# Kernel tuning notes

Measured on AMD Instinct MI355X. Metric: run time of the kernel, lower is better.

## Reference

```python
import jax, jax.numpy as jnp
import numpy as np
import math

B, T, C = 2, 2048, 768
NH, HD = 12, 64  # n_head, head_dim

def setup_inputs() -> dict:
    key = jax.random.key(0)
    k1, k2, k3 = jax.random.split(key, 3)
    x = jax.random.normal(k1, (B, T, C), dtype=jnp.float32)
    mask = jnp.tril(jnp.ones((T, T), dtype=bool))[None, None]  # [1,1,T,T] causal
    Wqkv = jax.random.normal(k2, (C, 3 * C), dtype=jnp.float32) * (1.0 / math.sqrt(C))
    Wproj = jax.random.normal(k3, (C, C), dtype=jnp.float32) * (1.0 / math.sqrt(C))
    return {"x": x, "mask": mask, "Wqkv": Wqkv, "Wproj": Wproj}

def reference(x, mask, Wqkv, Wproj):
    b, t, c = x.shape
    qkv = x @ Wqkv  # [b,t,3c]
    q, k, v = jnp.split(qkv, 3, axis=-1)
    q = q.reshape(b, t, NH, HD).transpose(0, 2, 1, 3)  # [b,h,t,d]
    k = k.reshape(b, t, NH, HD).transpose(0, 2, 1, 3)
    v = v.reshape(b, t, NH, HD).transpose(0, 2, 1, 3)
    att = jnp.einsum('bhqd,bhkd->bhqk', q, k) / math.sqrt(HD)
    att = jnp.where(mask, att, -jnp.inf)
    att = jax.nn.softmax(att, axis=-1)
    out = jnp.einsum('bhqk,bhkd->bhqd', att, v)
    out = out.transpose(0, 2, 1, 3).reshape(b, t, c)
    return out @ Wproj
```

## Files before the change

### kernel.cpp

```cpp
#include <hip/hip_runtime.h>
#include <hip/hip_bf16.h>

#define T_   2048
#define C_   768
#define NH_  12
#define HD_  64
#define M_   (2*T_)
#define N1_  (3*C_)
#define PB_  ((size_t)NH_*T_*HD_)
#define KS_  0.180336880f
#define MK_  8.65617024f

typedef __attribute__((ext_vector_type(8))) short  short8;
typedef __attribute__((ext_vector_type(4))) short  shortx4;
typedef __attribute__((ext_vector_type(4))) float  floatx4;

__device__ __forceinline__ floatx4 mfma_bf16(short8 a, short8 b, floatx4 c) {
    return __builtin_amdgcn_mfma_f32_16x16x32_bf16(a, b, c, 0, 0, 0);
}
__device__ __forceinline__ float fast_exp2(float x) {
    return __builtin_amdgcn_exp2f(x);
}
__device__ __forceinline__ void wave_fence() {
    __builtin_amdgcn_fence(__ATOMIC_SEQ_CST, "wavefront");
}
__device__ __forceinline__ void async_load16(const __hip_bfloat16* g, __hip_bfloat16* l) {
    __builtin_amdgcn_global_load_lds(
        (const __attribute__((address_space(1))) void*)g,
        (__attribute__((address_space(3))) void*)l, 16, 0, 0);
}

__global__ __launch_bounds__(256) void prep_all(const float* __restrict__ x,
                                                const float* __restrict__ wqkv,
                                                const float* __restrict__ wproj,
                                                __hip_bfloat16* __restrict__ xb,
                                                __hip_bfloat16* __restrict__ wqkvT,
                                                __hip_bfloat16* __restrict__ wprojT) {
    if (blockIdx.x < 3072) {
        const int idx = blockIdx.x * 256 + threadIdx.x;
        const floatx4 v = ((const floatx4*)x)[idx];
        union { __hip_bfloat16 h[4]; shortx4 s; } u;
#pragma unroll
        for (int j = 0; j < 4; j++) u.h[j] = __float2bfloat16(v[j]);
        ((shortx4*)xb)[idx] = u.s;
    } else if (blockIdx.x < 3936) {
        const int j  = (blockIdx.x - 3072) * 256 + threadIdx.x;
        const int k8 = j / N1_;
        const int n  = j - k8 * N1_;
        union { __hip_bfloat16 h[8]; short8 s; } u;
#pragma unroll
        for (int jj = 0; jj < 8; jj++)
            u.h[jj] = __float2bfloat16(wqkv[(size_t)(k8 * 8 + jj) * N1_ + n]);
        *(short8*)(wqkvT + (size_t)n * C_ + k8 * 8) = u.s;
    } else {
        const int j  = (blockIdx.x - 3936) * 256 + threadIdx.x;
        const int k8 = j / C_;
        const int n  = j - k8 * C_;
        union { __hip_bfloat16 h[8]; short8 s; } u;
#pragma unroll
        for (int jj = 0; jj < 8; jj++)
            u.h[jj] = __float2bfloat16(wproj[(size_t)(k8 * 8 + jj) * C_ + n]);
        *(short8*)(wprojT + (size_t)n * C_ + k8 * 8) = u.s;
    }
}

__global__ __launch_bounds__(256) void prep1(const float* __restrict__ x,
                                             const float* __restrict__ wqkv,
                                             __hip_bfloat16* __restrict__ xb,
                                             __hip_bfloat16* __restrict__ wqkvT) {
    if (blockIdx.x < 3072) {
        const int idx = blockIdx.x * 256 + threadIdx.x;
        const floatx4 v = ((const floatx4*)x)[idx];
        union { __hip_bfloat16 h[4]; shortx4 s; } u;
#pragma unroll
        for (int j = 0; j < 4; j++) u.h[j] = __float2bfloat16(v[j]);
        ((shortx4*)xb)[idx] = u.s;
    } else {
        const int j  = (blockIdx.x - 3072) * 256 + threadIdx.x;
        const int k8 = j / N1_;
        const int n  = j - k8 * N1_;
        union { __hip_bfloat16 h[8]; short8 s; } u;
#pragma unroll
        for (int jj = 0; jj < 8; jj++)
            u.h[jj] = __float2bfloat16(wqkv[(size_t)(k8 * 8 + jj) * N1_ + n]);
        *(short8*)(wqkvT + (size_t)n * C_ + k8 * 8) = u.s;
    }
}
__global__ __launch_bounds__(256) void prep2(const float* __restrict__ wproj,
                                             __hip_bfloat16* __restrict__ wprojT) {
    const int j  = blockIdx.x * 256 + threadIdx.x;
    const int k8 = j / C_;
    const int n  = j - k8 * C_;
    union { __hip_bfloat16 h[8]; short8 s; } u;
#pragma unroll
    for (int jj = 0; jj < 8; jj++)
        u.h[jj] = __float2bfloat16(wproj[(size_t)(k8 * 8 + jj) * C_ + n]);
    *(short8*)(wprojT + (size_t)n * C_ + k8 * 8) = u.s;
}

__global__ __launch_bounds__(256) void gemm_bt64x128(const __hip_bfloat16* __restrict__ A,
                                                     const __hip_bfloat16* __restrict__ Bt,
                                                     int N, int K,
                                                     __hip_bfloat16* __restrict__ O0,
                                                     __hip_bfloat16* __restrict__ O1,
                                                     __hip_bfloat16* __restrict__ O2) {
    __shared__ __align__(16) __hip_bfloat16 As[64 * 32];
    __shared__ __align__(16) __hip_bfloat16 Bs[128 * 32];

    const int tid  = threadIdx.x;
    const int n0   = blockIdx.x * 128;
    const int m0   = blockIdx.y * 64;
    const int wave = tid >> 6;
    const int ln   = tid & 63;
    const int l16  = ln & 15;
    const int q4   = ln >> 4;
    const int wm   = (wave >> 1) * 32;
    const int wn   = (wave & 1) * 64;

    const int lrow = ln >> 2;
    const int loct = (ln & 3) * 8;
    const __hip_bfloat16* ApD  = A  + (size_t)(m0 + wave * 16 + lrow) * K + loct;
    const __hip_bfloat16* BpD0 = Bt + (size_t)(n0 + (2 * wave)     * 16 + lrow) * K + loct;
    const __hip_bfloat16* BpD1 = Bt + (size_t)(n0 + (2 * wave + 1) * 16 + lrow) * K + loct;
    __hip_bfloat16* AsD  = As + wave * 512;
    __hip_bfloat16* BsD0 = Bs + (2 * wave) * 512;
    __hip_bfloat16* BsD1 = Bs + (2 * wave + 1) * 512;

    floatx4 acc[2][4];
#pragma unroll
    for (int i = 0; i < 2; i++)
#pragma unroll
        for (int j = 0; j < 4; j++) acc[i][j] = (floatx4){0.f, 0.f, 0.f, 0.f};

    for (int k0 = 0; k0 < K; k0 += 32) {
        __syncthreads();
        async_load16(ApD  + k0, AsD);
        async_load16(BpD0 + k0, BsD0);
        async_load16(BpD1 + k0, BsD1);
        __syncthreads();
        short8 af[2], bfr[4];
#pragma unroll
        for (int i = 0; i < 2; i++)
            af[i] = *(const short8*)(As + (wm + i * 16 + l16) * 32 + q4 * 8);
#pragma unroll
        for (int j = 0; j < 4; j++)
            bfr[j] = *(const short8*)(Bs + (wn + j * 16 + l16) * 32 + q4 * 8);
#pragma unroll
        for (int i = 0; i < 2; i++)
#pragma unroll
            for (int j = 0; j < 4; j++)
                acc[i][j] = mfma_bf16(af[i], bfr[j], acc[i][j]);
    }

#pragma unroll
    for (int i = 0; i < 2; i++) {
        const int mbase = m0 + wm + i * 16 + q4 * 4;
#pragma unroll
        for (int j = 0; j < 4; j++) {
            const int n = n0 + wn + j * 16 + l16;
            const int which = n / C_;
            const int rem   = n - which * C_;
            const int h     = rem >> 6;
            const int d     = rem & 63;
#pragma unroll
            for (int r = 0; r < 4; r++) {
                const int mm = mbase + r;
                const __hip_bfloat16 hv = __float2bfloat16(acc[i][j][r]);
                const int bh = (mm >> 11) * NH_ + h;
                const int t  = mm & (T_ - 1);
                if (which == 0)      O0[((size_t)bh * T_ + t) * HD_ + d] = hv;
                else if (which == 1) O1[((size_t)bh * T_ + t) * HD_ + d] = hv;
                else                 O2[((size_t)bh * HD_ + d) * T_ + t] = hv;
            }
        }
    }
}

__global__ __launch_bounds__(256) void gemm_bt64(const __hip_bfloat16* __restrict__ A,
                                                 const __hip_bfloat16* __restrict__ Bt,
                                                 int N, int K,
                                                 float* __restrict__ O0) {
    __shared__ __align__(16) __hip_bfloat16 As[64 * 40];
    __shared__ __align__(16) __hip_bfloat16 Bs[64 * 40];

    const int tid  = threadIdx.x;
    const int n0   = blockIdx.x * 64;
    const int m0   = blockIdx.y * 64;
    const int srow = tid >> 2;
    const int scol = (tid & 3) * 8;
    const int wave = tid >> 6;
    const int ln   = tid & 63;
    const int l16  = ln & 15;
    const int q4   = ln >> 4;
    const int wm   = (wave >> 1) * 32;
    const int wn   = (wave & 1) * 32;

    floatx4 acc[2][2];
#pragma unroll
    for (int i = 0; i < 2; i++)
#pragma unroll
        for (int j = 0; j < 2; j++) acc[i][j] = (floatx4){0.f, 0.f, 0.f, 0.f};

    const __hip_bfloat16* Ap = A  + (size_t)(m0 + srow) * K + scol;
    const __hip_bfloat16* Bp = Bt + (size_t)(n0 + srow) * K + scol;

    for (int k0 = 0; k0 < K; k0 += 32) {
        short8 av = *(const short8*)(Ap + k0);
        short8 bv = *(const short8*)(Bp + k0);
        __syncthreads();
        *(short8*)(As + srow * 40 + scol) = av;
        *(short8*)(Bs + srow * 40 + scol) = bv;
        __syncthreads();
        short8 af[2], bfr[2];
#pragma unroll
        for (int i = 0; i < 2; i++) {
            af[i]  = *(const short8*)(As + (wm + i * 16 + l16) * 40 + q4 * 8);
            bfr[i] = *(const short8*)(Bs + (wn + i * 16 + l16) * 40 + q4 * 8);
        }
#pragma unroll
        for (int i = 0; i < 2; i++)
#pragma unroll
            for (int j = 0; j < 2; j++)
                acc[i][j] = mfma_bf16(af[i], bfr[j], acc[i][j]);
    }

#pragma unroll
    for (int i = 0; i < 2; i++) {
        const int mbase = m0 + wm + i * 16 + q4 * 4;
#pragma unroll
        for (int j = 0; j < 2; j++) {
            const int n = n0 + wn + j * 16 + l16;
#pragma unroll
            for (int r = 0; r < 4; r++)
                O0[(size_t)(mbase + r) * N + n] = acc[i][j][r];
        }
    }
}

__global__ __launch_bounds__(256) void attn_fused(const __hip_bfloat16* __restrict__ Q,
                                                  const __hip_bfloat16* __restrict__ Kd,
                                                  const __hip_bfloat16* __restrict__ Vt,
                                                  __hip_bfloat16* __restrict__ O) {
    __shared__ __align__(16) __hip_bfloat16 plds[4][2][16][72];

    const int bh   = blockIdx.x;
    const int wid  = threadIdx.x >> 6;
    const int lane = threadIdx.x & 63;
    const int l16  = lane & 15;
    const int q4   = lane >> 4;
    const int i    = 63 - (int)blockIdx.y;
    const int q0A  = 32 * i;
    const int q0B  = 32 * i + 16;
    const int nch  = (i >> 1) + 1;

    const __hip_bfloat16* Qh = Q  + (size_t)bh * T_ * HD_;
    const __hip_bfloat16* Kh = Kd + (size_t)bh * T_ * HD_;
    const __hip_bfloat16* Vh = Vt + (size_t)bh * HD_ * T_;

    short8 aqA[2], aqB[2];
#pragma unroll
    for (int kt = 0; kt < 2; kt++) {
        aqA[kt] = *(const short8*)(Qh + (size_t)(q0A + l16) * HD_ + kt * 32 + q4 * 8);
        aqB[kt] = *(const short8*)(Qh + (size_t)(q0B + l16) * HD_ + kt * 32 + q4 * 8);
    }

    floatx4 accA[4], accB[4];
#pragma unroll
    for (int ct = 0; ct < 4; ct++) {
        accA[ct] = (floatx4){0.f, 0.f, 0.f, 0.f};
        accB[ct] = (floatx4){0.f, 0.f, 0.f, 0.f};
    }
    float lsA[4] = {0.f, 0.f, 0.f, 0.f};
    float lsB[4] = {0.f, 0.f, 0.f, 0.f};

    for (int c = wid; c < nch; c += 4) {
        const int kv0 = c * 64;
        const bool diag = (c == nch - 1);

        short8 bk[4][2];
#pragma unroll
        for (int nt = 0; nt < 4; nt++)
#pragma unroll
            for (int kt = 0; kt < 2; kt++)
                bk[nt][kt] = *(const short8*)(Kh + (size_t)(kv0 + nt * 16 + l16) * HD_ + kt * 32 + q4 * 8);

        floatx4 sA[4], sB[4];
#pragma unroll
        for (int nt = 0; nt < 4; nt++) {
            sA[nt] = (floatx4){0.f, 0.f, 0.f, 0.f};
            sB[nt] = (floatx4){0.f, 0.f, 0.f, 0.f};
#pragma unroll
            for (int kt = 0; kt < 2; kt++) {
                sA[nt] = mfma_bf16(aqA[kt], bk[nt][kt], sA[nt]);
                sB[nt] = mfma_bf16(aqB[kt], bk[nt][kt], sB[nt]);
            }
        }

        if (diag) {
#pragma unroll
            for (int r = 0; r < 4; r++) {
#pragma unroll
                for (int nt = 0; nt < 4; nt++) {
                    const int kvc = kv0 + nt * 16 + l16;
                    if (kvc > q0A + q4 * 4 + r) sA[nt][r] = -3e38f;
                    if (kvc > q0B + q4 * 4 + r) sB[nt][r] = -3e38f;
                }
            }
        }

#pragma unroll
        for (int r = 0; r < 4; r++) {
            float ra = 0.f, rb = 0.f;
#pragma unroll
            for (int nt = 0; nt < 4; nt++) {
                const float pa = fast_exp2(sA[nt][r] * KS_ - MK_);
                const float pb = fast_exp2(sB[nt][r] * KS_ - MK_);
                plds[wid][0][q4 * 4 + r][nt * 16 + l16] = __float2bfloat16(pa);
                plds[wid][1][q4 * 4 + r][nt * 16 + l16] = __float2bfloat16(pb);
                ra += pa; rb += pb;
            }
            lsA[r] += ra; lsB[r] += rb;
        }

        wave_fence();

        short8 apA[2], apB[2];
#pragma unroll
        for (int kt = 0; kt < 2; kt++) {
            apA[kt] = *(const short8*)(&plds[wid][0][l16][kt * 32 + q4 * 8]);
            apB[kt] = *(const short8*)(&plds[wid][1][l16][kt * 32 + q4 * 8]);
        }
#pragma unroll
        for (int ct = 0; ct < 4; ct++)
#pragma unroll
            for (int kt = 0; kt < 2; kt++) {
                short8 bv = *(const short8*)(Vh + (size_t)(ct * 16 + l16) * T_ + kv0 + kt * 32 + q4 * 8);
                accA[ct] = mfma_bf16(apA[kt], bv, accA[ct]);
                accB[ct] = mfma_bf16(apB[kt], bv, accB[ct]);
            }

        wave_fence();
    }

#pragma unroll
    for (int off = 1; off < 16; off <<= 1)
#pragma unroll
        for (int r = 0; r < 4; r++) {
            lsA[r] += __shfl_xor(lsA[r], off, 64);
            lsB[r] += __shfl_xor(lsB[r], off, 64);
        }

    __syncthreads();
    floatx4* accbuf = (floatx4*)&plds[0][0][0][0];
    float*   lbuf   = (float*)((char*)&plds[0][0][0][0] + 16384);

    auto publish = [&](int slot) {
#pragma unroll
        for (int ct = 0; ct < 4; ct++) {
            accbuf[((slot * 2 + 0) * 4 + ct) * 64 + lane] = accA[ct];
            accbuf[((slot * 2 + 1) * 4 + ct) * 64 + lane] = accB[ct];
        }
        if (l16 == 0) {
#pragma unroll
            for (int r = 0; r < 4; r++) {
                lbuf[(slot * 2 + 0) * 16 + q4 * 4 + r] = lsA[r];
                lbuf[(slot * 2 + 1) * 16 + q4 * 4 + r] = lsB[r];
            }
        }
    };
    auto mergeIn = [&](int slot) {
#pragma unroll
        for (int ct = 0; ct < 4; ct++) {
            accA[ct] += accbuf[((slot * 2 + 0) * 4 + ct) * 64 + lane];
            accB[ct] += accbuf[((slot * 2 + 1) * 4 + ct) * 64 + lane];
        }
#pragma unroll
        for (int r = 0; r < 4; r++) {
            lsA[r] += lbuf[(slot * 2 + 0) * 16 + q4 * 4 + r];
            lsB[r] += lbuf[(slot * 2 + 1) * 16 + q4 * 4 + r];
        }
    };

    if (wid >= 2) publish(wid - 2);
    __syncthreads();
    if (wid < 2) mergeIn(wid);
    __syncthreads();
    if (wid == 1) publish(0);
    __syncthreads();
    if (wid == 0) {
        mergeIn(0);
        const int orow0 = (bh / NH_) * T_;
        const int hcol  = (bh % NH_) * HD_;
#pragma unroll
        for (int r = 0; r < 4; r++) {
            const float invA = 1.0f / lsA[r];
            const float invB = 1.0f / lsB[r];
            __hip_bfloat16* oA = O + (size_t)(orow0 + q0A + q4 * 4 + r) * C_ + hcol;
            __hip_bfloat16* oB = O + (size_t)(orow0 + q0B + q4 * 4 + r) * C_ + hcol;
#pragma unroll
            for (int ct = 0; ct < 4; ct++) {
                oA[ct * 16 + l16] = __float2bfloat16(accA[ct][r] * invA);
                oB[ct * 16 + l16] = __float2bfloat16(accB[ct][r] * invB);
            }
        }
    }
}

extern "C" void kernel_launch(void* const* d_in, const int* in_sizes, int n_in,
                              void* d_out, int out_size, void* d_ws, size_t ws_size,
                              hipStream_t stream) {
    const float *x = nullptr, *wqkv = nullptr, *wproj = nullptr;
    for (int i = 0; i < n_in; i++) {
        const int s = in_sizes[i];
        if (s == M_ * C_ && !x) x = (const float*)d_in[i];
        else if (s == C_ * N1_ && !wqkv) wqkv = (const float*)d_in[i];
        else if (s == C_ * C_ && !wproj) wproj = (const float*)d_in[i];
    }
    float* out = (float*)d_out;
    __hip_bfloat16* ws = (__hip_bfloat16*)d_ws;
    __hip_bfloat16* Vt = (__hip_bfloat16*)d_out;

    __hip_bfloat16* Qall  = ws;
    __hip_bfloat16* Kall  = Qall + 2 * PB_;
    __hip_bfloat16* ATT   = Kall + 2 * PB_;
    __hip_bfloat16* xb    = ATT;
    __hip_bfloat16* wqkvT = (__hip_bfloat16*)d_out + 2 * PB_;

    const size_t needMerged = (6 * PB_ + (size_t)C_ * C_) * sizeof(__hip_bfloat16);
    if (ws_size >= needMerged) {
        __hip_bfloat16* wprojT = ws + 6 * PB_;
        prep_all<<<dim3(4224), 256, 0, stream>>>(x, wqkv, wproj, xb, wqkvT, wprojT);
        gemm_bt64x128<<<dim3(N1_ / 128, M_ / 64), 256, 0, stream>>>(
            xb, wqkvT, N1_, C_, Qall, Kall, Vt);
        attn_fused<<<dim3(2 * NH_, 64), 256, 0, stream>>>(Qall, Kall, Vt, ATT);
        gemm_bt64<<<dim3(C_ / 64, M_ / 64), 256, 0, stream>>>(ATT, wprojT, C_, C_, out);
    } else {
        __hip_bfloat16* wprojT = Qall;
        prep1<<<dim3(3936), 256, 0, stream>>>(x, wqkv, xb, wqkvT);
        gemm_bt64x128<<<dim3(N1_ / 128, M_ / 64), 256, 0, stream>>>(
            xb, wqkvT, N1_, C_, Qall, Kall, Vt);
        attn_fused<<<dim3(2 * NH_, 64), 256, 0, stream>>>(Qall, Kall, Vt, ATT);
        prep2<<<dim3(288), 256, 0, stream>>>(wproj, wprojT);
        gemm_bt64<<<dim3(C_ / 64, M_ / 64), 256, 0, stream>>>(ATT, wprojT, C_, C_, out);
    }
}
```

Baseline: 194.3 us.

## Transpose QK^T MFMA operands to pack P stores and hoist V loads

Swaps the A/B operands of the score MFMA so each lane holds four consecutive key columns for a single query row. That lets P be written to LDS as packed 4-element bf16 vectors instead of scalar stores. It also shrinks the row-sum to one scalar per lane, reduced with two cross-lane shuffles instead of a 4-step butterfly. V loads are hoisted to the top of each chunk next to the K loads to overlap their latency with the QK MFMAs, at the cost of more live registers.

```diff
diff --git a/kernel.cpp b/kernel.cpp
--- a/kernel.cpp
+++ b/kernel.cpp
@@ -270,8 +270,7 @@
         accA[ct] = (floatx4){0.f, 0.f, 0.f, 0.f};
         accB[ct] = (floatx4){0.f, 0.f, 0.f, 0.f};
     }
-    float lsA[4] = {0.f, 0.f, 0.f, 0.f};
-    float lsB[4] = {0.f, 0.f, 0.f, 0.f};
+    float sumA = 0.f, sumB = 0.f;
 
     for (int c = wid; c < nch; c += 4) {
         const int kv0 = c * 64;
@@ -284,6 +283,13 @@
             for (int kt = 0; kt < 2; kt++)
                 bk[nt][kt] = *(const short8*)(Kh + (size_t)(kv0 + nt * 16 + l16) * HD_ + kt * 32 + q4 * 8);
 
+        short8 bv[4][2];
+#pragma unroll
+        for (int ct = 0; ct < 4; ct++)
+#pragma unroll
+            for (int kt = 0; kt < 2; kt++)
+                bv[ct][kt] = *(const short8*)(Vh + (size_t)(ct * 16 + l16) * T_ + kv0 + kt * 32 + q4 * 8);
+
         floatx4 sA[4], sB[4];
 #pragma unroll
         for (int nt = 0; nt < 4; nt++) {
@@ -291,35 +297,38 @@
             sB[nt] = (floatx4){0.f, 0.f, 0.f, 0.f};
 #pragma unroll
             for (int kt = 0; kt < 2; kt++) {
-                sA[nt] = mfma_bf16(aqA[kt], bk[nt][kt], sA[nt]);
-                sB[nt] = mfma_bf16(aqB[kt], bk[nt][kt], sB[nt]);
+                sA[nt] = mfma_bf16(bk[nt][kt], aqA[kt], sA[nt]);
+                sB[nt] = mfma_bf16(bk[nt][kt], aqB[kt], sB[nt]);
             }
         }
 
         if (diag) {
 #pragma unroll
+            for (int nt = 0; nt < 4; nt++) {
+#pragma unroll
+                for (int r = 0; r < 4; r++) {
+                    const int kvg = kv0 + nt * 16 + q4 * 4 + r;
+                    if (kvg > q0A + l16) sA[nt][r] = -3e38f;
+                    if (kvg > q0B + l16) sB[nt][r] = -3e38f;
+                }
+            }
+        }
+
+#pragma unroll
+        for (int nt = 0; nt < 4; nt++) {
+            union { __hip_bfloat16 h[4]; shortx4 s; } uA, uB;
+            float pA[4], pB[4];
+#pragma unroll
             for (int r = 0; r < 4; r++) {
-#pragma unroll
-                for (int nt = 0; nt < 4; nt++) {
-                    const int kvc = kv0 + nt * 16 + l16;
-                    if (kvc > q0A + q4 * 4 + r) sA[nt][r] = -3e38f;
-                    if (kvc > q0B + q4 * 4 + r) sB[nt][r] = -3e38f;
-                }
-            }
-        }
-
-#pragma unroll
-        for (int r = 0; r < 4; r++) {
-            float ra = 0.f, rb = 0.f;
-#pragma unroll
-            for (int nt = 0; nt < 4; nt++) {
-                const float pa = fast_exp2(sA[nt][r] * KS_ - MK_);
-                const float pb = fast_exp2(sB[nt][r] * KS_ - MK_);
-                plds[wid][0][q4 * 4 + r][nt * 16 + l16] = __float2bfloat16(pa);
-                plds[wid][1][q4 * 4 + r][nt * 16 + l16] = __float2bfloat16(pb);
-                ra += pa; rb += pb;
-            }
-            lsA[r] += ra; lsB[r] += rb;
+                pA[r] = fast_exp2(sA[nt][r] * KS_ - MK_);
+                pB[r] = fast_exp2(sB[nt][r] * KS_ - MK_);
+                uA.h[r] = __float2bfloat16(pA[r]);
+                uB.h[r] = __float2bfloat16(pB[r]);
+            }
+            sumA += (pA[0] + pA[1]) + (pA[2] + pA[3]);
+            sumB += (pB[0] + pB[1]) + (pB[2] + pB[3]);
+            *(shortx4*)(&plds[wid][0][l16][nt * 16 + q4 * 4]) = uA.s;
+            *(shortx4*)(&plds[wid][1][l16][nt * 16 + q4 * 4]) = uB.s;
         }
 
         wave_fence();
@@ -334,21 +343,17 @@
         for (int ct = 0; ct < 4; ct++)
 #pragma unroll
             for (int kt = 0; kt < 2; kt++) {
-                short8 bv = *(const short8*)(Vh + (size_t)(ct * 16 + l16) * T_ + kv0 + kt * 32 + q4 * 8);
-                accA[ct] = mfma_bf16(apA[kt], bv, accA[ct]);
-                accB[ct] = mfma_bf16(apB[kt], bv, accB[ct]);
+                accA[ct] = mfma_bf16(apA[kt], bv[ct][kt], accA[ct]);
+                accB[ct] = mfma_bf16(apB[kt], bv[ct][kt], accB[ct]);
             }
 
         wave_fence();
     }
 
-#pragma unroll
-    for (int off = 1; off < 16; off <<= 1)
-#pragma unroll
-        for (int r = 0; r < 4; r++) {
-            lsA[r] += __shfl_xor(lsA[r], off, 64);
-            lsB[r] += __shfl_xor(lsB[r], off, 64);
-        }
+    sumA += __shfl_xor(sumA, 16, 64);
+    sumA += __shfl_xor(sumA, 32, 64);
+    sumB += __shfl_xor(sumB, 16, 64);
+    sumB += __shfl_xor(sumB, 32, 64);
 
     __syncthreads();
     floatx4* accbuf = (floatx4*)&plds[0][0][0][0];
@@ -360,12 +365,9 @@
             accbuf[((slot * 2 + 0) * 4 + ct) * 64 + lane] = accA[ct];
             accbuf[((slot * 2 + 1) * 4 + ct) * 64 + lane] = accB[ct];
         }
-        if (l16 == 0) {
-#pragma unroll
-            for (int r = 0; r < 4; r++) {
-                lbuf[(slot * 2 + 0) * 16 + q4 * 4 + r] = lsA[r];
-                lbuf[(slot * 2 + 1) * 16 + q4 * 4 + r] = lsB[r];
-            }
+        if (q4 == 0) {
+            lbuf[(slot * 2 + 0) * 16 + l16] = sumA;
+            lbuf[(slot * 2 + 1) * 16 + l16] = sumB;
         }
     };
     auto mergeIn = [&](int slot) {
@@ -374,11 +376,8 @@
             accA[ct] += accbuf[((slot * 2 + 0) * 4 + ct) * 64 + lane];
             accB[ct] += accbuf[((slot * 2 + 1) * 4 + ct) * 64 + lane];
         }
-#pragma unroll
-        for (int r = 0; r < 4; r++) {
-            lsA[r] += lbuf[(slot * 2 + 0) * 16 + q4 * 4 + r];
-            lsB[r] += lbuf[(slot * 2 + 1) * 16 + q4 * 4 + r];
-        }
+        sumA += lbuf[(slot * 2 + 0) * 16 + l16];
+        sumB += lbuf[(slot * 2 + 1) * 16 + l16];
     };
 
     if (wid >= 2) publish(wid - 2);
@@ -393,8 +392,8 @@
         const int hcol  = (bh % NH_) * HD_;
 #pragma unroll
         for (int r = 0; r < 4; r++) {
-            const float invA = 1.0f / lsA[r];
-            const float invB = 1.0f / lsB[r];
+            const float invA = 1.0f / __shfl(sumA, q4 * 4 + r, 64);
+            const float invB = 1.0f / __shfl(sumB, q4 * 4 + r, 64);
             __hip_bfloat16* oA = O + (size_t)(orow0 + q0A + q4 * 4 + r) * C_ + hcol;
             __hip_bfloat16* oB = O + (size_t)(orow0 + q0B + q4 * 4 + r) * C_ + hcol;
 #pragma unroll
```

New measurement: 193.9 us. Within noise of the previous version (-0.2%).
